# Performance work log

Measured on AMD Instinct MI355X. Metric: run time of the kernel, lower is better.

## Reference

```python
import jax, jax.numpy as jnp
import numpy as np
import math

N_HEADS = 16


def _rope(t, cos, sin):
    # t: [B, S, H, d_k] with d_k paired as (even, odd) -> complex multiply by cos+i*sin
    B, S, H, dk = t.shape
    t = t.reshape(B, S, H, dk // 2, 2)
    t0, t1 = t[..., 0], t[..., 1]
    c = cos[None, :S, None, :]
    s = sin[None, :S, None, :]
    out = jnp.stack([t0 * c - t1 * s, t0 * s + t1 * c], axis=-1)
    return out.reshape(B, S, H, dk)


def setup_inputs() -> dict:
    key = jax.random.key(0)
    ks = jax.random.split(key, 6)
    B, S, D = 2, 2048, 2048
    dk = D // N_HEADS  # 128
    x = jax.random.normal(ks[0], (B, S, D), dtype=jnp.float32)
    # standard RoPE angle table
    inv_freq = 1.0 / (10000.0 ** (np.arange(0, dk, 2, dtype=np.float32) / dk))  # [dk/2]
    t = np.arange(S, dtype=np.float32)
    ang = np.outer(t, inv_freq)  # [S, dk/2]
    freqs_cos = jnp.asarray(np.cos(ang), dtype=jnp.float32)
    freqs_sin = jnp.asarray(np.sin(ang), dtype=jnp.float32)
    # additive causal mask [1,1,S,S]
    causal = jnp.tril(jnp.ones((S, S), dtype=bool))
    mask = jnp.where(causal, 0.0, -1e9).astype(jnp.float32)[None, None]
    wscale = 1.0 / math.sqrt(D)
    Wq = jax.random.normal(ks[1], (D, D), dtype=jnp.float32) * wscale
    Wk = jax.random.normal(ks[2], (D, D), dtype=jnp.float32) * wscale
    Wv = jax.random.normal(ks[3], (D, D), dtype=jnp.float32) * wscale
    Wo = jax.random.normal(ks[4], (D, D), dtype=jnp.float32) * wscale
    return {"x": x, "freqs_cos": freqs_cos, "freqs_sin": freqs_sin, "mask": mask,
            "Wq": Wq, "Wk": Wk, "Wv": Wv, "Wo": Wo}


def reference(x, freqs_cos, freqs_sin, mask, Wq, Wk, Wv, Wo):
    B, S, D = x.shape
    H = N_HEADS
    dk = D // H
    scale = math.sqrt(dk)
    # nn.Linear(w) applies x @ w.T
    Q = (x @ Wq.T).reshape(B, S, H, dk)
    K = (x @ Wk.T).reshape(B, S, H, dk)
    V = (x @ Wv.T).reshape(B, S, H, dk)
    Q = _rope(Q, freqs_cos, freqs_sin)
    K = _rope(K, freqs_cos, freqs_sin)
    new_kv_cache = (K, V)  # kv_cache=None path: cache is just current K, V
    # [B, H, S, dk]
    Qh = Q.transpose(0, 2, 1, 3)
    Kh = K.transpose(0, 2, 1, 3)
    Vh = V.transpose(0, 2, 1, 3)
    scores = jnp.einsum('bhqd,bhkd->bhqk', Qh, Kh) / scale + mask
    attn = jax.nn.softmax(scores, axis=-1)  # dropout=0 (eval)
    ctx = jnp.einsum('bhqk,bhkd->bhqd', attn, Vh)
    ctx = ctx.transpose(0, 2, 1, 3).reshape(B, S, D)
    output = ctx @ Wo.T
    return output, new_kv_cache[0], new_kv_cache[1]
```

## Files before the change

kernel.cpp:

```cpp
#include <hip/hip_runtime.h>
#include <hip/hip_bf16.h>

#define SEQ   2048
#define DIM   2048
#define NH    16
#define DKH   128
#define BATCH 2
#define MROWS (BATCH * SEQ)
#define NQT   (SEQ / 64)

using bf16 = __hip_bfloat16;
typedef __attribute__((ext_vector_type(8))) short short8;
typedef __attribute__((ext_vector_type(4))) short short4v;
typedef __attribute__((ext_vector_type(4))) float floatx4;

union BfBits { bf16 h; short s; };

__device__ __forceinline__ void gl_lds16(const bf16* g, bf16* l) {
  __builtin_amdgcn_global_load_lds(
      (__attribute__((address_space(1))) void*)(g),
      (__attribute__((address_space(3))) void*)(l), 16, 0, 0);
}

#define S_BAR  __builtin_amdgcn_s_barrier()
#define VMCNT6 do { asm volatile("s_waitcnt vmcnt(6)" ::: "memory"); __builtin_amdgcn_sched_barrier(0); } while (0)
#define VMCNT0 do { asm volatile("s_waitcnt vmcnt(0)" ::: "memory"); __builtin_amdgcn_sched_barrier(0); } while (0)
#define LGKM0  do { asm volatile("s_waitcnt lgkmcnt(0)" ::: "memory"); __builtin_amdgcn_sched_barrier(0); } while (0)

__global__ __launch_bounds__(256) void cast5_kernel(const float* __restrict__ x,
                                                    const float* __restrict__ wq,
                                                    const float* __restrict__ wk,
                                                    const float* __restrict__ wv,
                                                    const float* __restrict__ wo,
                                                    bf16* __restrict__ dst,
                                                    int nX4, int nW4, int nTot) {
  int i = blockIdx.x * 256 + threadIdx.x;
  if (i >= nTot) return;
  const float* src;
  int off;
  int j = i - nX4;
  if (j < 0) { src = x; off = i; }
  else {
    int wsel = j >> 20;
    off = j & (nW4 - 1);
    src = (wsel == 0) ? wq : (wsel == 1) ? wk : (wsel == 2) ? wv : wo;
  }
  float4 v = reinterpret_cast<const float4*>(src)[off];
  __hip_bfloat162 h01, h23;
  h01.x = __float2bfloat16(v.x); h01.y = __float2bfloat16(v.y);
  h23.x = __float2bfloat16(v.z); h23.y = __float2bfloat16(v.w);
  reinterpret_cast<__hip_bfloat162*>(dst)[i * 2 + 0] = h01;
  reinterpret_cast<__hip_bfloat162*>(dst)[i * 2 + 1] = h23;
}

#define BUFE (256 * 64 + 128 * 64)

template <int ROWS>
__device__ __forceinline__ void stage_swz(const bf16* __restrict__ G, bf16* lds,
                                          int row0, int k0, int w, int l) {
  const int rr = w * 8 + (l >> 3);
  const int cc = ((l & 7) * 8) ^ ((l >> 3) * 8);
#pragma unroll
  for (int u = 0; u < ROWS / 64; ++u)
    gl_lds16(G + (size_t)(row0 + u * 64 + rr) * DIM + k0 + cc,
             lds + (u * 64 + w * 8) * 64);
}

template <int MODE>
__global__ __launch_bounds__(512, 2) void gemm256(const bf16* __restrict__ A,
                                                  const bf16* __restrict__ Bw,
                                                  bf16* __restrict__ Qraw,
                                                  float* __restrict__ Kout,
                                                  float* __restrict__ Vout) {
  __shared__ bf16 smem[3 * BUFE];

  const int t = threadIdx.x;
  const int w = t >> 6, l = t & 63;
  const int lr = l & 15, quad = l >> 4;
  const int wr = w >> 2;
  const int wc = w & 3;
  const int m0 = blockIdx.y * 256;
  const int n0g = blockIdx.x * 128;

  const int cb = ((quad * 8) ^ ((lr & 7) * 8));

  floatx4 acc[8][2];
#pragma unroll
  for (int mi = 0; mi < 8; ++mi)
#pragma unroll
    for (int nj = 0; nj < 2; ++nj) acc[mi][nj] = (floatx4){0.f, 0.f, 0.f, 0.f};

  const int NT = DIM / 64;

  stage_swz<256>(A, smem, m0, 0, w, l);
  stage_swz<128>(Bw, smem + 256 * 64, n0g, 0, w, l);
  stage_swz<256>(A, smem + BUFE, m0, 64, w, l);
  stage_swz<128>(Bw, smem + BUFE + 256 * 64, n0g, 64, w, l);
  VMCNT6;
  S_BAR;

  for (int kt = 0; kt < NT; ++kt) {
    const bf16* la = smem + (kt % 3) * BUFE;
    const bf16* lb = la + 256 * 64;
    bf16* stg = smem + ((kt + 2) % 3) * BUFE;
    const bool do_stage = (kt + 2 < NT);

    short8 bfr[2][2];
#pragma unroll
    for (int nj = 0; nj < 2; ++nj) {
      int rb = (wc * 32 + nj * 16 + lr) * 64;
      bfr[nj][0] = *reinterpret_cast<const short8*>(lb + rb + cb);
      bfr[nj][1] = *reinterpret_cast<const short8*>(lb + rb + (cb ^ 32));
    }
    short8 af[4][2];
#pragma unroll
    for (int i = 0; i < 4; ++i) {
      int ra = (wr * 128 + i * 16 + lr) * 64;
      af[i][0] = *reinterpret_cast<const short8*>(la + ra + cb);
      af[i][1] = *reinterpret_cast<const short8*>(la + ra + (cb ^ 32));
    }
    if (do_stage) stage_swz<256>(A, stg, m0, (kt + 2) * 64, w, l);
    LGKM0;
    __builtin_amdgcn_s_setprio(1);
#pragma unroll
    for (int i = 0; i < 4; ++i)
#pragma unroll
      for (int nj = 0; nj < 2; ++nj) {
        acc[i][nj] = __builtin_amdgcn_mfma_f32_16x16x32_bf16(
            af[i][0], bfr[nj][0], acc[i][nj], 0, 0, 0);
        acc[i][nj] = __builtin_amdgcn_mfma_f32_16x16x32_bf16(
            af[i][1], bfr[nj][1], acc[i][nj], 0, 0, 0);
      }
    __builtin_amdgcn_s_setprio(0);

#pragma unroll
    for (int i = 0; i < 4; ++i) {
      int ra = (wr * 128 + (i + 4) * 16 + lr) * 64;
      af[i][0] = *reinterpret_cast<const short8*>(la + ra + cb);
      af[i][1] = *reinterpret_cast<const short8*>(la + ra + (cb ^ 32));
    }
    if (do_stage) stage_swz<128>(Bw, stg + 256 * 64, n0g, (kt + 2) * 64, w, l);
    LGKM0;
    __builtin_amdgcn_s_setprio(1);
#pragma unroll
    for (int i = 0; i < 4; ++i)
#pragma unroll
      for (int nj = 0; nj < 2; ++nj) {
        acc[i + 4][nj] = __builtin_amdgcn_mfma_f32_16x16x32_bf16(
            af[i][0], bfr[nj][0], acc[i + 4][nj], 0, 0, 0);
        acc[i + 4][nj] = __builtin_amdgcn_mfma_f32_16x16x32_bf16(
            af[i][1], bfr[nj][1], acc[i + 4][nj], 0, 0, 0);
      }
    __builtin_amdgcn_s_setprio(0);

    if (do_stage) { VMCNT6; } else { VMCNT0; }
    S_BAR;
  }

#pragma unroll
  for (int mi = 0; mi < 8; ++mi)
#pragma unroll
    for (int nj = 0; nj < 2; ++nj) {
      int rg = m0 + wr * 128 + mi * 16 + quad * 4;
      if constexpr (MODE == 0) {
        const int region = n0g >> 11;
        int lcol = (n0g & 2047) + wc * 32 + nj * 16 + lr;
#pragma unroll
        for (int rr2 = 0; rr2 < 4; ++rr2) {
          size_t idx = (size_t)(rg + rr2) * DIM + lcol;
          if (region == 0)      Qraw[idx] = __float2bfloat16(acc[mi][nj][rr2]);
          else if (region == 1) Kout[idx] = acc[mi][nj][rr2];
          else                  Vout[idx] = acc[mi][nj][rr2];
        }
      } else {
        int lcol = n0g + wc * 32 + nj * 16 + lr;
#pragma unroll
        for (int rr2 = 0; rr2 < 4; ++rr2)
          Kout[(size_t)(rg + rr2) * DIM + lcol] = acc[mi][nj][rr2];
      }
    }
}

#define NRB ((MROWS * DIM / 2) / 256)

__global__ __launch_bounds__(256) void postproc(const bf16* __restrict__ Qraw,
                                                float* __restrict__ Kf,
                                                const float* __restrict__ cosT,
                                                const float* __restrict__ sinT,
                                                bf16* __restrict__ Qb,
                                                bf16* __restrict__ Kb,
                                                const float* __restrict__ V,
                                                bf16* __restrict__ Vt) {
  int bid = blockIdx.x;
  if (bid < NRB) {
    int g = bid * 256 + threadIdx.x;
    int p = g & 63;
    int r = g >> 6;
    int h = r & 15;
    int s = (r >> 4) & (SEQ - 1);
    int b = r >> 15;
    __hip_bfloat162 v = reinterpret_cast<const __hip_bfloat162*>(Qraw)[g];
    float x0 = __bfloat162float(v.x), x1 = __bfloat162float(v.y);
    float c = cosT[s * 64 + p], sn = sinT[s * 64 + p];
    __hip_bfloat162 o;
    o.x = __float2bfloat16(x0 * c - x1 * sn);
    o.y = __float2bfloat16(x0 * sn + x1 * c);
    reinterpret_cast<__hip_bfloat162*>(Qb)[((size_t)(b * NH + h) * SEQ + s) * 64 + p] = o;
    return;
  }
  bid -= NRB;
  if (bid < NRB) {
    int g = bid * 256 + threadIdx.x;
    int p = g & 63;
    int r = g >> 6;
    int h = r & 15;
    int s = (r >> 4) & (SEQ - 1);
    int b = r >> 15;
    float2 v = reinterpret_cast<const float2*>(Kf)[g];
    float c = cosT[s * 64 + p], sn = sinT[s * 64 + p];
    float o0 = v.x * c - v.y * sn;
    float o1 = v.x * sn + v.y * c;
    reinterpret_cast<float2*>(Kf)[g] = make_float2(o0, o1);
    __hip_bfloat162 ob;
    ob.x = __float2bfloat16(o0);
    ob.y = __float2bfloat16(o1);
    reinterpret_cast<__hip_bfloat162*>(Kb)[((size_t)(b * NH + h) * SEQ + s) * 64 + p] = ob;
    return;
  }
  bid -= NRB;
  {
    __shared__ float tile[32][33];
    const int s0 = (bid & 63) * 32;
    const int d0 = ((bid >> 6) & 3) * 32;
    const int bh = bid >> 8;
    const int b = bh >> 4, h = bh & 15;
    const int t = threadIdx.x;
    const int row = t >> 3, c4 = (t & 7) * 4;

    float4 v = *reinterpret_cast<const float4*>(
        V + (size_t)(b * SEQ + s0 + row) * DIM + h * DKH + d0 + c4);
    tile[row][c4 + 0] = v.x; tile[row][c4 + 1] = v.y;
    tile[row][c4 + 2] = v.z; tile[row][c4 + 3] = v.w;
    __syncthreads();

    short4v ov;
#pragma unroll
    for (int i = 0; i < 4; ++i) {
      BfBits u; u.h = __float2bfloat16(tile[c4 + i][row]);
      ov[i] = u.s;
    }
    *reinterpret_cast<short4v*>(Vt + ((size_t)(b * NH + h) * DKH + d0 + row) * SEQ + s0 + c4) = ov;
  }
}

__global__ __launch_bounds__(256) void attn_mfma(const bf16* __restrict__ Qb,
                                                 const bf16* __restrict__ Kb,
                                                 const bf16* __restrict__ Vt,
                                                 bf16* __restrict__ ctx) {
  const int bx = blockIdx.x;
  const int h = blockIdx.y;
  const int b = blockIdx.z;
  const int t = threadIdx.x;
  const int w = t >> 6, lane = t & 63;
  const int lr = lane & 15, quad = lane >> 4;
  const int kswz = 8 * (lr & 7);

  __shared__ short Ks[2][64 * 128];
  __shared__ short Vs[2][128 * 64];
  __shared__ short Ps[4 * 16 * 72];

  const float scale2 = 0.08838834764831845f * 1.44269504f;
  const float THR = 11.5413f;
  const size_t headQK = (size_t)(b * NH + h) * SEQ * DKH;
  const short* kbase0 = (const short*)Kb + headQK;
  const short* vbase0 = (const short*)Vt + (size_t)(b * NH + h) * DKH * SEQ;

  const int krow_l = w * 4 + (lane >> 4);
  const int kcol_l = ((lane & 15) * 8) ^ (8 * (krow_l & 7));
  const int vrow_l = w * 8 + (lane >> 3);
  const int vcol_l = ((lane & 7) * 8) ^ (8 * (vrow_l & 7));

  auto STAGE = [&](int kt, int buf) {
#pragma unroll
    for (int u = 0; u < 4; ++u) {
      gl_lds16((const bf16*)(kbase0 + (size_t)(kt * 64 + krow_l + 16 * u) * DKH + kcol_l),
               (bf16*)(&Ks[buf][(w * 64 + 256 * u) * 8]));
      gl_lds16((const bf16*)(vbase0 + (size_t)(vrow_l + 32 * u) * SEQ + kt * 64 + vcol_l),
               (bf16*)(&Vs[buf][(w * 64 + 256 * u) * 8]));
    }
  };

  for (int pass = 0; pass < 2; ++pass) {
    const int qt = pass ? bx : (NQT - 1 - bx);

    short8 qa[4];
    {
      const short* qbase = (const short*)Qb + headQK + (size_t)(qt * 64 + w * 16 + lr) * DKH;
#pragma unroll
      for (int kk = 0; kk < 4; ++kk)
        qa[kk] = *reinterpret_cast<const short8*>(qbase + kk * 32 + quad * 8);
    }

    floatx4 o[8];
#pragma unroll
    for (int n = 0; n < 8; ++n) o[n] = (floatx4){0.f, 0.f, 0.f, 0.f};
    float m[4] = {-1e30f, -1e30f, -1e30f, -1e30f};
    float l[4] = {0.f, 0.f, 0.f, 0.f};

    STAGE(0, 0);
    __syncthreads();

    for (int kt = 0; kt <= qt; ++kt) {
      const int cur = kt & 1;
      if (kt < qt) STAGE(kt + 1, cur ^ 1);
      const short* ksb = Ks[cur];
      const short* vsb = Vs[cur];

      floatx4 sj[4];
#pragma unroll
      for (int j = 0; j < 4; ++j) sj[j] = (floatx4){0.f, 0.f, 0.f, 0.f};
#pragma unroll
      for (int j = 0; j < 4; ++j)
#pragma unroll
        for (int kk = 0; kk < 4; ++kk) {
          short8 kb = *reinterpret_cast<const short8*>(
              ksb + (j * 16 + lr) * 128 + ((kk * 32 + quad * 8) ^ kswz));
          sj[j] = __builtin_amdgcn_mfma_f32_16x16x32_bf16(qa[kk], kb, sj[j], 0, 0, 0);
        }

      float sc[4][4];
#pragma unroll
      for (int j = 0; j < 4; ++j)
#pragma unroll
        for (int r = 0; r < 4; ++r) sc[j][r] = sj[j][r] * scale2;
      if (kt == qt) {
#pragma unroll
        for (int j = 0; j < 4; ++j) {
          int col = kt * 64 + j * 16 + lr;
#pragma unroll
          for (int r = 0; r < 4; ++r) {
            int rowg = qt * 64 + w * 16 + quad * 4 + r;
            if (col > rowg) sc[j][r] = -1e9f;
          }
        }
      }

#pragma unroll
      for (int r = 0; r < 4; ++r) {
        float mx = fmaxf(fmaxf(sc[0][r], sc[1][r]), fmaxf(sc[2][r], sc[3][r]));
        mx = fmaxf(mx, __shfl_xor(mx, 1, 16));
        mx = fmaxf(mx, __shfl_xor(mx, 2, 16));
        mx = fmaxf(mx, __shfl_xor(mx, 4, 16));
        mx = fmaxf(mx, __shfl_xor(mx, 8, 16));
        if (!__all(mx - m[r] <= THR)) {
          float mnew = fmaxf(m[r], mx);
          float alpha = __builtin_amdgcn_exp2f(m[r] - mnew);
          l[r] *= alpha;
#pragma unroll
          for (int n = 0; n < 8; ++n) o[n][r] *= alpha;
          m[r] = mnew;
        }
        float rs = 0.f;
#pragma unroll
        for (int j = 0; j < 4; ++j) {
          float p = __builtin_amdgcn_exp2f(sc[j][r] - m[r]);
          rs += p;
          BfBits u; u.h = __float2bfloat16(p);
          Ps[(w * 16 + quad * 4 + r) * 72 + j * 16 + lr] = u.s;
        }
        rs += __shfl_xor(rs, 1, 16);
        rs += __shfl_xor(rs, 2, 16);
        rs += __shfl_xor(rs, 4, 16);
        rs += __shfl_xor(rs, 8, 16);
        l[r] += rs;
      }

      short8 pa0 = *reinterpret_cast<const short8*>(Ps + (w * 16 + lr) * 72 + quad * 8);
      short8 pa1 = *reinterpret_cast<const short8*>(Ps + (w * 16 + lr) * 72 + 32 + quad * 8);
#pragma unroll
      for (int n = 0; n < 8; ++n) {
        short8 vb0 = *reinterpret_cast<const short8*>(
            vsb + (n * 16 + lr) * 64 + ((quad * 8) ^ kswz));
        short8 vb1 = *reinterpret_cast<const short8*>(
            vsb + (n * 16 + lr) * 64 + ((32 + quad * 8) ^ kswz));
        o[n] = __builtin_amdgcn_mfma_f32_16x16x32_bf16(pa0, vb0, o[n], 0, 0, 0);
        o[n] = __builtin_amdgcn_mfma_f32_16x16x32_bf16(pa1, vb1, o[n], 0, 0, 0);
      }
      __syncthreads();
    }

    float inv[4];
#pragma unroll
    for (int r = 0; r < 4; ++r) inv[r] = 1.0f / l[r];
#pragma unroll
    for (int r = 0; r < 4; ++r) {
      size_t mrow = (size_t)b * SEQ + qt * 64 + w * 16 + quad * 4 + r;
      bf16* dst = ctx + mrow * DIM + h * DKH;
#pragma unroll
      for (int n = 0; n < 8; ++n)
        dst[n * 16 + lr] = __float2bfloat16(o[n][r] * inv[r]);
    }
  }
}

extern "C" void kernel_launch(void* const* d_in, const int* in_sizes, int n_in,
                              void* d_out, int out_size, void* d_ws, size_t ws_size,
                              hipStream_t stream) {
  const float* x = (const float*)d_in[0];
  const float* fcos = (const float*)d_in[1];
  const float* fsin = (const float*)d_in[2];
  const float* Wq = (const float*)d_in[4];
  const float* Wk = (const float*)d_in[5];
  const float* Wv = (const float*)d_in[6];
  const float* Wo = (const float*)d_in[7];

  float* out = (float*)d_out;
  float* Kout = out + (size_t)MROWS * DIM;
  float* Vout = Kout + (size_t)MROWS * DIM;

  const size_t MD = (size_t)MROWS * DIM;
  const size_t DD = (size_t)DIM * DIM;
  bf16* xb   = (bf16*)d_ws;
  bf16* Wqb  = xb + MD;
  bf16* Wkb  = Wqb + DD;
  bf16* Wvb  = Wkb + DD;
  bf16* Wob  = Wvb + DD;
  bf16* Qraw = Wob + DD;
  bf16* Qb   = Qraw + MD;
  bf16* Kb   = Qb + MD;
  bf16* Vt   = Kb + MD;
  bf16* ctxb = Qraw;

  const int nXD4 = MROWS * DIM / 4;
  const int nWD4 = DIM * DIM / 4;
  const int nTot = nXD4 + 4 * nWD4;
  cast5_kernel<<<nTot / 256, 256, 0, stream>>>(x, Wq, Wk, Wv, Wo, xb, nXD4, nWD4, nTot);

  dim3 gq(3 * DIM / 128, MROWS / 256);
  gemm256<0><<<gq, 512, 0, stream>>>(xb, Wqb, Qraw, Kout, Vout);

  postproc<<<2 * NRB + 8192, 256, 0, stream>>>(Qraw, Kout, fcos, fsin, Qb, Kb, Vout, Vt);

  dim3 ga(NQT / 2, NH, BATCH);
  attn_mfma<<<ga, 256, 0, stream>>>(Qb, Kb, Vt, ctxb);

  dim3 go(DIM / 128, MROWS / 256);
  gemm256<1><<<go, 512, 0, stream>>>(ctxb, Wob, (bf16*)nullptr, out, (float*)nullptr);
}
```

Before: 458.5 us.

## Fuse RoPE, head-major relayout and V transpose into QKV GEMM epilogue

Removes the separate postproc kernel. The QKV GEMM epilogue now applies RoPE to Q and K using lane shuffles to pair adjacent columns, writes head-major bf16 Q/K plus fp32 K output, and transposes V through shared memory into Vt. This saves a launch and a round trip of Qraw/K/V through global memory. In exchange the epilogue gets scattered cos/sin loads and 2-byte strided stores, and the ctx buffer now gets its own workspace region instead of reusing Qraw.

```diff
diff --git a/kernel.cpp b/kernel.cpp
--- a/kernel.cpp
+++ b/kernel.cpp
@@ -11,7 +11,6 @@
 
 using bf16 = __hip_bfloat16;
 typedef __attribute__((ext_vector_type(8))) short short8;
-typedef __attribute__((ext_vector_type(4))) short short4v;
 typedef __attribute__((ext_vector_type(4))) float floatx4;
 
 union BfBits { bf16 h; short s; };
@@ -69,9 +68,14 @@
 template <int MODE>
 __global__ __launch_bounds__(512, 2) void gemm256(const bf16* __restrict__ A,
                                                   const bf16* __restrict__ Bw,
-                                                  bf16* __restrict__ Qraw,
+                                                  bf16* __restrict__ Qb,
+                                                  bf16* __restrict__ Kb,
                                                   float* __restrict__ Kout,
-                                                  float* __restrict__ Vout) {
+                                                  float* __restrict__ Vout,
+                                                  bf16* __restrict__ Vt,
+                                                  const float* __restrict__ cosT,
+                                                  const float* __restrict__ sinT,
+                                                  float* __restrict__ Cout) {
   __shared__ bf16 smem[3 * BUFE];
 
   const int t = threadIdx.x;
@@ -157,99 +161,78 @@
     S_BAR;
   }
 
-#pragma unroll
-  for (int mi = 0; mi < 8; ++mi)
-#pragma unroll
-    for (int nj = 0; nj < 2; ++nj) {
-      int rg = m0 + wr * 128 + mi * 16 + quad * 4;
-      if constexpr (MODE == 0) {
-        const int region = n0g >> 11;
-        int lcol = (n0g & 2047) + wc * 32 + nj * 16 + lr;
-#pragma unroll
-        for (int rr2 = 0; rr2 < 4; ++rr2) {
-          size_t idx = (size_t)(rg + rr2) * DIM + lcol;
-          if (region == 0)      Qraw[idx] = __float2bfloat16(acc[mi][nj][rr2]);
-          else if (region == 1) Kout[idx] = acc[mi][nj][rr2];
-          else                  Vout[idx] = acc[mi][nj][rr2];
-        }
-      } else {
+  if constexpr (MODE == 1) {
+#pragma unroll
+    for (int mi = 0; mi < 8; ++mi)
+#pragma unroll
+      for (int nj = 0; nj < 2; ++nj) {
+        int rg = m0 + wr * 128 + mi * 16 + quad * 4;
         int lcol = n0g + wc * 32 + nj * 16 + lr;
 #pragma unroll
         for (int rr2 = 0; rr2 < 4; ++rr2)
-          Kout[(size_t)(rg + rr2) * DIM + lcol] = acc[mi][nj][rr2];
-      }
-    }
-}
-
-#define NRB ((MROWS * DIM / 2) / 256)
-
-__global__ __launch_bounds__(256) void postproc(const bf16* __restrict__ Qraw,
-                                                float* __restrict__ Kf,
-                                                const float* __restrict__ cosT,
-                                                const float* __restrict__ sinT,
-                                                bf16* __restrict__ Qb,
-                                                bf16* __restrict__ Kb,
-                                                const float* __restrict__ V,
-                                                bf16* __restrict__ Vt) {
-  int bid = blockIdx.x;
-  if (bid < NRB) {
-    int g = bid * 256 + threadIdx.x;
-    int p = g & 63;
-    int r = g >> 6;
-    int h = r & 15;
-    int s = (r >> 4) & (SEQ - 1);
-    int b = r >> 15;
-    __hip_bfloat162 v = reinterpret_cast<const __hip_bfloat162*>(Qraw)[g];
-    float x0 = __bfloat162float(v.x), x1 = __bfloat162float(v.y);
-    float c = cosT[s * 64 + p], sn = sinT[s * 64 + p];
-    __hip_bfloat162 o;
-    o.x = __float2bfloat16(x0 * c - x1 * sn);
-    o.y = __float2bfloat16(x0 * sn + x1 * c);
-    reinterpret_cast<__hip_bfloat162*>(Qb)[((size_t)(b * NH + h) * SEQ + s) * 64 + p] = o;
-    return;
-  }
-  bid -= NRB;
-  if (bid < NRB) {
-    int g = bid * 256 + threadIdx.x;
-    int p = g & 63;
-    int r = g >> 6;
-    int h = r & 15;
-    int s = (r >> 4) & (SEQ - 1);
-    int b = r >> 15;
-    float2 v = reinterpret_cast<const float2*>(Kf)[g];
-    float c = cosT[s * 64 + p], sn = sinT[s * 64 + p];
-    float o0 = v.x * c - v.y * sn;
-    float o1 = v.x * sn + v.y * c;
-    reinterpret_cast<float2*>(Kf)[g] = make_float2(o0, o1);
-    __hip_bfloat162 ob;
-    ob.x = __float2bfloat16(o0);
-    ob.y = __float2bfloat16(o1);
-    reinterpret_cast<__hip_bfloat162*>(Kb)[((size_t)(b * NH + h) * SEQ + s) * 64 + p] = ob;
-    return;
-  }
-  bid -= NRB;
-  {
-    __shared__ float tile[32][33];
-    const int s0 = (bid & 63) * 32;
-    const int d0 = ((bid >> 6) & 3) * 32;
-    const int bh = bid >> 8;
-    const int b = bh >> 4, h = bh & 15;
-    const int t = threadIdx.x;
-    const int row = t >> 3, c4 = (t & 7) * 4;
-
-    float4 v = *reinterpret_cast<const float4*>(
-        V + (size_t)(b * SEQ + s0 + row) * DIM + h * DKH + d0 + c4);
-    tile[row][c4 + 0] = v.x; tile[row][c4 + 1] = v.y;
-    tile[row][c4 + 2] = v.z; tile[row][c4 + 3] = v.w;
-    __syncthreads();
-
-    short4v ov;
-#pragma unroll
-    for (int i = 0; i < 4; ++i) {
-      BfBits u; u.h = __float2bfloat16(tile[c4 + i][row]);
-      ov[i] = u.s;
-    }
-    *reinterpret_cast<short4v*>(Vt + ((size_t)(b * NH + h) * DKH + d0 + row) * SEQ + s0 + c4) = ov;
+          Cout[(size_t)(rg + rr2) * DIM + lcol] = acc[mi][nj][rr2];
+      }
+  } else {
+    const int region = n0g >> 11;
+    const int h = (n0g & 2047) >> 7;
+    if (region < 2) {
+#pragma unroll
+      for (int mi = 0; mi < 8; ++mi)
+#pragma unroll
+        for (int nj = 0; nj < 2; ++nj) {
+          const int rbase = m0 + wr * 128 + mi * 16 + quad * 4;
+          const int d = wc * 32 + nj * 16 + lr;
+          const int p = d >> 1;
+#pragma unroll
+          for (int rr2 = 0; rr2 < 4; ++rr2) {
+            int row = rbase + rr2;
+            int s = row & (SEQ - 1), bb = row >> 11;
+            float v = acc[mi][nj][rr2];
+            float prt = __shfl_xor(v, 1);
+            float c = cosT[s * 64 + p], sn = sinT[s * 64 + p];
+            float o = (lr & 1) ? (prt * sn + v * c) : (v * c - prt * sn);
+            size_t idx = ((size_t)(bb * NH + h) * SEQ + s) * DKH + d;
+            if (region == 0) {
+              Qb[idx] = __float2bfloat16(o);
+            } else {
+              Kb[idx] = __float2bfloat16(o);
+              Kout[(size_t)row * DIM + h * DKH + d] = o;
+            }
+          }
+        }
+    } else {
+      short* T = reinterpret_cast<short*>(smem);
+#pragma unroll
+      for (int mi = 0; mi < 8; ++mi)
+#pragma unroll
+        for (int nj = 0; nj < 2; ++nj) {
+          const int d = wc * 32 + nj * 16 + lr;
+          const int rl = wr * 128 + mi * 16 + quad * 4;
+          const int rbase = m0 + rl;
+#pragma unroll
+          for (int rr2 = 0; rr2 < 4; ++rr2)
+            Vout[(size_t)(rbase + rr2) * DIM + h * DKH + d] = acc[mi][nj][rr2];
+          BfBits b0, b1, b2, b3;
+          b0.h = __float2bfloat16(acc[mi][nj][0]);
+          b1.h = __float2bfloat16(acc[mi][nj][1]);
+          b2.h = __float2bfloat16(acc[mi][nj][2]);
+          b3.h = __float2bfloat16(acc[mi][nj][3]);
+          unsigned u0 = (unsigned short)b0.s | ((unsigned)(unsigned short)b1.s << 16);
+          unsigned u1 = (unsigned short)b2.s | ((unsigned)(unsigned short)b3.s << 16);
+          *reinterpret_cast<unsigned*>(&T[d * 268 + rl]) = u0;
+          *reinterpret_cast<unsigned*>(&T[d * 268 + rl + 2]) = u1;
+        }
+      __syncthreads();
+      const int d2 = t >> 2, sq = t & 3;
+      const int s0 = m0 & (SEQ - 1);
+      const int bb = m0 >> 11;
+      short* vtp = (short*)Vt + ((size_t)(bb * NH + h) * DKH + d2) * SEQ + s0 + sq * 64;
+#pragma unroll
+      for (int u = 0; u < 16; ++u) {
+        int2 val = *reinterpret_cast<const int2*>(&T[d2 * 268 + sq * 64 + u * 4]);
+        *reinterpret_cast<int2*>(vtp + u * 4) = val;
+      }
+    }
   }
 }
 
@@ -425,11 +408,10 @@
   bf16* Wkb  = Wqb + DD;
   bf16* Wvb  = Wkb + DD;
   bf16* Wob  = Wvb + DD;
-  bf16* Qraw = Wob + DD;
-  bf16* Qb   = Qraw + MD;
+  bf16* Qb   = Wob + DD;
   bf16* Kb   = Qb + MD;
   bf16* Vt   = Kb + MD;
-  bf16* ctxb = Qraw;
+  bf16* ctxb = Vt + MD;
 
   const int nXD4 = MROWS * DIM / 4;
   const int nWD4 = DIM * DIM / 4;
@@ -437,13 +419,14 @@
   cast5_kernel<<<nTot / 256, 256, 0, stream>>>(x, Wq, Wk, Wv, Wo, xb, nXD4, nWD4, nTot);
 
   dim3 gq(3 * DIM / 128, MROWS / 256);
-  gemm256<0><<<gq, 512, 0, stream>>>(xb, Wqb, Qraw, Kout, Vout);
-
-  postproc<<<2 * NRB + 8192, 256, 0, stream>>>(Qraw, Kout, fcos, fsin, Qb, Kb, Vout, Vt);
+  gemm256<0><<<gq, 512, 0, stream>>>(xb, Wqb, Qb, Kb, Kout, Vout, Vt, fcos, fsin,
+                                     (float*)nullptr);
 
   dim3 ga(NQT / 2, NH, BATCH);
   attn_mfma<<<ga, 256, 0, stream>>>(Qb, Kb, Vt, ctxb);
 
   dim3 go(DIM / 128, MROWS / 256);
-  gemm256<1><<<go, 512, 0, stream>>>(ctxb, Wob, (bf16*)nullptr, out, (float*)nullptr);
-}
+  gemm256<1><<<go, 512, 0, stream>>>(ctxb, Wob, (bf16*)nullptr, (bf16*)nullptr,
+                                     (float*)nullptr, (float*)nullptr, (bf16*)nullptr,
+                                     (const float*)nullptr, (const float*)nullptr, out);
+}
```

Result: no change. 458.5 us (+0.0%).

## Split GEMM main loop into four barrier-separated phases and remap attention blocks across XCDs

Applied to the files above, without the earlier changes.

The GEMM inner loop now runs four phases of two A-row fragments each instead of two phases of four. Global-to-LDS staging chunks are spread across the phases, and extra workgroup barriers are added so waves interleave MFMA work with loads in lockstep. This also lowers A-fragment register pressure. The attention kernel switches to a 1D grid with a block-index swizzle so that neighbouring logical tiles (same head) land on the same XCD, which should improve L2 reuse of K/V. The added barriers may cost some stall time.

```diff
diff --git a/kernel.cpp b/kernel.cpp
--- a/kernel.cpp
+++ b/kernel.cpp
@@ -55,15 +55,12 @@
 
 #define BUFE (256 * 64 + 128 * 64)
 
-template <int ROWS>
-__device__ __forceinline__ void stage_swz(const bf16* __restrict__ G, bf16* lds,
-                                          int row0, int k0, int w, int l) {
+__device__ __forceinline__ void stage_chunk(const bf16* __restrict__ G, bf16* lds,
+                                            int row0, int k0, int w, int l, int u) {
   const int rr = w * 8 + (l >> 3);
   const int cc = ((l & 7) * 8) ^ ((l >> 3) * 8);
-#pragma unroll
-  for (int u = 0; u < ROWS / 64; ++u)
-    gl_lds16(G + (size_t)(row0 + u * 64 + rr) * DIM + k0 + cc,
-             lds + (u * 64 + w * 8) * 64);
+  gl_lds16(G + (size_t)(row0 + u * 64 + rr) * DIM + k0 + cc,
+           lds + (u * 64 + w * 8) * 64);
 }
 
 template <int MODE>
@@ -92,67 +89,111 @@
 
   const int NT = DIM / 64;
 
-  stage_swz<256>(A, smem, m0, 0, w, l);
-  stage_swz<128>(Bw, smem + 256 * 64, n0g, 0, w, l);
-  stage_swz<256>(A, smem + BUFE, m0, 64, w, l);
-  stage_swz<128>(Bw, smem + BUFE + 256 * 64, n0g, 64, w, l);
+#pragma unroll
+  for (int u = 0; u < 4; ++u) stage_chunk(A, smem, m0, 0, w, l, u);
+#pragma unroll
+  for (int u = 0; u < 2; ++u) stage_chunk(Bw, smem + 256 * 64, n0g, 0, w, l, u);
+#pragma unroll
+  for (int u = 0; u < 4; ++u) stage_chunk(A, smem + BUFE, m0, 64, w, l, u);
+#pragma unroll
+  for (int u = 0; u < 2; ++u) stage_chunk(Bw, smem + BUFE + 256 * 64, n0g, 64, w, l, u);
   VMCNT6;
   S_BAR;
 
   for (int kt = 0; kt < NT; ++kt) {
     const bf16* la = smem + (kt % 3) * BUFE;
     const bf16* lb = la + 256 * 64;
-    bf16* stg = smem + ((kt + 2) % 3) * BUFE;
+    bf16* stgA = smem + ((kt + 2) % 3) * BUFE;
+    bf16* stgB = stgA + 256 * 64;
+    const int k2 = (kt + 2) * 64;
     const bool do_stage = (kt + 2 < NT);
 
     short8 bfr[2][2];
+    short8 af[2][2];
+
 #pragma unroll
     for (int nj = 0; nj < 2; ++nj) {
       int rb = (wc * 32 + nj * 16 + lr) * 64;
       bfr[nj][0] = *reinterpret_cast<const short8*>(lb + rb + cb);
       bfr[nj][1] = *reinterpret_cast<const short8*>(lb + rb + (cb ^ 32));
     }
-    short8 af[4][2];
-#pragma unroll
-    for (int i = 0; i < 4; ++i) {
+#pragma unroll
+    for (int i = 0; i < 2; ++i) {
       int ra = (wr * 128 + i * 16 + lr) * 64;
       af[i][0] = *reinterpret_cast<const short8*>(la + ra + cb);
       af[i][1] = *reinterpret_cast<const short8*>(la + ra + (cb ^ 32));
     }
-    if (do_stage) stage_swz<256>(A, stg, m0, (kt + 2) * 64, w, l);
+    if (do_stage) { stage_chunk(A, stgA, m0, k2, w, l, 0); stage_chunk(A, stgA, m0, k2, w, l, 1); }
+    S_BAR;
     LGKM0;
     __builtin_amdgcn_s_setprio(1);
 #pragma unroll
-    for (int i = 0; i < 4; ++i)
+    for (int i = 0; i < 2; ++i)
 #pragma unroll
       for (int nj = 0; nj < 2; ++nj) {
-        acc[i][nj] = __builtin_amdgcn_mfma_f32_16x16x32_bf16(
-            af[i][0], bfr[nj][0], acc[i][nj], 0, 0, 0);
-        acc[i][nj] = __builtin_amdgcn_mfma_f32_16x16x32_bf16(
-            af[i][1], bfr[nj][1], acc[i][nj], 0, 0, 0);
+        acc[i][nj] = __builtin_amdgcn_mfma_f32_16x16x32_bf16(af[i][0], bfr[nj][0], acc[i][nj], 0, 0, 0);
+        acc[i][nj] = __builtin_amdgcn_mfma_f32_16x16x32_bf16(af[i][1], bfr[nj][1], acc[i][nj], 0, 0, 0);
       }
     __builtin_amdgcn_s_setprio(0);
-
-#pragma unroll
-    for (int i = 0; i < 4; ++i) {
+    S_BAR;
+
+#pragma unroll
+    for (int i = 0; i < 2; ++i) {
+      int ra = (wr * 128 + (i + 2) * 16 + lr) * 64;
+      af[i][0] = *reinterpret_cast<const short8*>(la + ra + cb);
+      af[i][1] = *reinterpret_cast<const short8*>(la + ra + (cb ^ 32));
+    }
+    if (do_stage) { stage_chunk(A, stgA, m0, k2, w, l, 2); stage_chunk(A, stgA, m0, k2, w, l, 3); }
+    S_BAR;
+    LGKM0;
+    __builtin_amdgcn_s_setprio(1);
+#pragma unroll
+    for (int i = 0; i < 2; ++i)
+#pragma unroll
+      for (int nj = 0; nj < 2; ++nj) {
+        acc[i + 2][nj] = __builtin_amdgcn_mfma_f32_16x16x32_bf16(af[i][0], bfr[nj][0], acc[i + 2][nj], 0, 0, 0);
+        acc[i + 2][nj] = __builtin_amdgcn_mfma_f32_16x16x32_bf16(af[i][1], bfr[nj][1], acc[i + 2][nj], 0, 0, 0);
+      }
+    __builtin_amdgcn_s_setprio(0);
+    S_BAR;
+
+#pragma unroll
+    for (int i = 0; i < 2; ++i) {
       int ra = (wr * 128 + (i + 4) * 16 + lr) * 64;
       af[i][0] = *reinterpret_cast<const short8*>(la + ra + cb);
       af[i][1] = *reinterpret_cast<const short8*>(la + ra + (cb ^ 32));
     }
-    if (do_stage) stage_swz<128>(Bw, stg + 256 * 64, n0g, (kt + 2) * 64, w, l);
+    if (do_stage) { stage_chunk(Bw, stgB, n0g, k2, w, l, 0); stage_chunk(Bw, stgB, n0g, k2, w, l, 1); }
+    S_BAR;
     LGKM0;
     __builtin_amdgcn_s_setprio(1);
 #pragma unroll
-    for (int i = 0; i < 4; ++i)
+    for (int i = 0; i < 2; ++i)
 #pragma unroll
       for (int nj = 0; nj < 2; ++nj) {
-        acc[i + 4][nj] = __builtin_amdgcn_mfma_f32_16x16x32_bf16(
-            af[i][0], bfr[nj][0], acc[i + 4][nj], 0, 0, 0);
-        acc[i + 4][nj] = __builtin_amdgcn_mfma_f32_16x16x32_bf16(
-            af[i][1], bfr[nj][1], acc[i + 4][nj], 0, 0, 0);
+        acc[i + 4][nj] = __builtin_amdgcn_mfma_f32_16x16x32_bf16(af[i][0], bfr[nj][0], acc[i + 4][nj], 0, 0, 0);
+        acc[i + 4][nj] = __builtin_amdgcn_mfma_f32_16x16x32_bf16(af[i][1], bfr[nj][1], acc[i + 4][nj], 0, 0, 0);
       }
     __builtin_amdgcn_s_setprio(0);
-
+    S_BAR;
+
+#pragma unroll
+    for (int i = 0; i < 2; ++i) {
+      int ra = (wr * 128 + (i + 6) * 16 + lr) * 64;
+      af[i][0] = *reinterpret_cast<const short8*>(la + ra + cb);
+      af[i][1] = *reinterpret_cast<const short8*>(la + ra + (cb ^ 32));
+    }
+    S_BAR;
+    LGKM0;
+    __builtin_amdgcn_s_setprio(1);
+#pragma unroll
+    for (int i = 0; i < 2; ++i)
+#pragma unroll
+      for (int nj = 0; nj < 2; ++nj) {
+        acc[i + 6][nj] = __builtin_amdgcn_mfma_f32_16x16x32_bf16(af[i][0], bfr[nj][0], acc[i + 6][nj], 0, 0, 0);
+        acc[i + 6][nj] = __builtin_amdgcn_mfma_f32_16x16x32_bf16(af[i][1], bfr[nj][1], acc[i + 6][nj], 0, 0, 0);
+      }
+    __builtin_amdgcn_s_setprio(0);
     if (do_stage) { VMCNT6; } else { VMCNT0; }
     S_BAR;
   }
@@ -257,9 +298,11 @@
                                                  const bf16* __restrict__ Kb,
                                                  const bf16* __restrict__ Vt,
                                                  bf16* __restrict__ ctx) {
-  const int bx = blockIdx.x;
-  const int h = blockIdx.y;
-  const int b = blockIdx.z;
+  const int orig = blockIdx.x;
+  const int logical = (orig & 7) * 64 + (orig >> 3);
+  const int bx = logical & 15;
+  const int h = (logical >> 4) & 15;
+  const int b = logical >> 8;
   const int t = threadIdx.x;
   const int w = t >> 6, lane = t & 63;
   const int lr = lane & 15, quad = lane >> 4;
@@ -441,8 +484,7 @@
 
   postproc<<<2 * NRB + 8192, 256, 0, stream>>>(Qraw, Kout, fcos, fsin, Qb, Kb, Vout, Vt);
 
-  dim3 ga(NQT / 2, NH, BATCH);
-  attn_mfma<<<ga, 256, 0, stream>>>(Qb, Kb, Vt, ctxb);
+  attn_mfma<<<512, 256, 0, stream>>>(Qb, Kb, Vt, ctxb);
 
   dim3 go(DIM / 128, MROWS / 256);
   gemm256<1><<<go, 512, 0, stream>>>(ctxb, Wob, (bf16*)nullptr, out, (float*)nullptr);
```

After: 464.4 us. No clear change (+1.3%).
